# Performance work log

Hardware: AMD Instinct MI355X
Metric: run time of the kernel (lower is better)

Reference implementation:

```python
import jax, jax.numpy as jnp
import numpy as np

HIDDEN = 32
N_STEPS = 64  # fixed-step RK4 replaces adaptive Dopri5 (same MLP-eval structure)
STD = 0.1     # init_params: Linear weights ~ N(0, 0.1), biases = 0


def _mlp(w1, b1, w2, b2, w3, b3, y):
    # NODE.forward: fc1 -> relu -> fc2 -> relu -> fc3 (t is unused in the source)
    h = jax.nn.relu(y @ w1 + b1)
    h = jax.nn.relu(h @ w2 + b2)
    return h @ w3 + b3


def setup_inputs() -> dict:
    key = jax.random.key(0)
    ks = jax.random.split(key, 8)
    B, D = 131072, 3
    x = jax.random.normal(ks[0], (B, D), dtype=jnp.float32)
    # eval times in (0.1, 1.0], sorted like a posterior-sample schedule
    samples = jnp.sort(
        jax.random.uniform(ks[1], (8, 1), jnp.float32, 0.1, 1.0), axis=0)
    w1 = (STD * jax.random.normal(ks[2], (D, HIDDEN))).astype(jnp.float32)
    b1 = jnp.zeros((HIDDEN,), jnp.float32)
    w2 = (STD * jax.random.normal(ks[3], (HIDDEN, HIDDEN))).astype(jnp.float32)
    b2 = jnp.zeros((HIDDEN,), jnp.float32)
    w3 = (STD * jax.random.normal(ks[4], (HIDDEN, D))).astype(jnp.float32)
    b3 = jnp.zeros((D,), jnp.float32)
    w_out = (STD * jax.random.normal(ks[5], (D, 1))).astype(jnp.float32)
    b_out = jnp.zeros((1,), jnp.float32)
    return {"x": x, "samples": samples, "w1": w1, "b1": b1, "w2": w2,
            "b2": b2, "w3": w3, "b3": b3, "w_out": w_out, "b_out": b_out}


def reference(x, samples, w1, b1, w2, b2, w3, b3, w_out, b_out):
    t_eval = samples[:, 0]                     # (S,)
    max_T = jnp.max(t_eval)
    dt = max_T / N_STEPS

    def step(y, _):
        k1 = _mlp(w1, b1, w2, b2, w3, b3, y)
        k2 = _mlp(w1, b1, w2, b2, w3, b3, y + 0.5 * dt * k1)
        k3 = _mlp(w1, b1, w2, b2, w3, b3, y + 0.5 * dt * k2)
        k4 = _mlp(w1, b1, w2, b2, w3, b3, y + dt * k3)
        y_new = y + (dt / 6.0) * (k1 + 2.0 * k2 + 2.0 * k3 + k4)
        return y_new, y_new

    # traj[i] is the state at time (i+1)*dt; shape (N_STEPS, B, 3)
    _, traj = jax.lax.scan(jax.checkpoint(step), x, jnp.arange(N_STEPS))

    # gather states at the grid step nearest each eval time
    idx = jnp.clip(jnp.round(t_eval / dt).astype(jnp.int32) - 1, 0, N_STEPS - 1)
    y_eval = traj[idx]                         # (S, B, 3)

    # fc_layers readout -> act_vec (S, B, 1)
    return y_eval @ w_out + b_out
```

## Files before the change

kernel.cpp:

```cpp
#include <hip/hip_runtime.h>

#define NSTEPS 64

typedef __attribute__((ext_vector_type(16))) float float16_;
typedef __attribute__((ext_vector_type(2))) __fp16 half2_;
typedef __attribute__((ext_vector_type(8))) __fp16 half8_;

__device__ __forceinline__ half2_ relu_pk_f16(float a, float b) {
    half2_ h = __builtin_amdgcn_cvt_pkrtz(a, b);
    return __builtin_elementwise_max(h, (half2_)(__fp16)0);
}

__global__ __launch_bounds__(256, 3)
void ode_rk4_mfma(const float* __restrict__ x,
                  const float* __restrict__ samples,
                  const float* __restrict__ w1, const float* __restrict__ b1,
                  const float* __restrict__ w2, const float* __restrict__ b2,
                  const float* __restrict__ w3, const float* __restrict__ b3,
                  const float* __restrict__ w_out, const float* __restrict__ b_out,
                  float* __restrict__ out, int B)
{
    const int lane  = threadIdx.x & 63;
    const int w     = threadIdx.x >> 6;
    const int col32 = lane & 31;
    const int half  = lane >> 5;

    const int rowBase = (blockIdx.x * 4 + w) * 32;
    const int row = rowBase + col32;

    auto pi = [](int m) -> int {
        int bb = (m >> 2) & 3;
        return m + ((bb == 1) ? 4 : (bb == 2) ? -4 : 0);
    };

    union { half2_ h2[4]; half8_ h8; } A1;
    {
        int pm = pi(col32);
        if (half == 0) {
            A1.h2[0] = (half2_){(__fp16)w1[0 * 32 + pm], (__fp16)w1[1 * 32 + pm]};
            A1.h2[1] = (half2_){(__fp16)w1[2 * 32 + pm], (__fp16)b1[pm]};
        } else {
            A1.h2[0] = (half2_)(__fp16)0.0f;
            A1.h2[1] = (half2_)(__fp16)0.0f;
        }
        A1.h2[2] = (half2_)(__fp16)0.0f;
        A1.h2[3] = (half2_)(__fp16)0.0f;
    }

    union { half2_ h2[4]; half8_ h8; } W2T1, W2T2;
#pragma unroll
    for (int pp = 0; pp < 4; ++pp) {
        int i1 = half * 8 + 2 * pp;
        W2T1.h2[pp] = (half2_){(__fp16)w2[i1 * 32 + col32], (__fp16)w2[(i1 + 1) * 32 + col32]};
        W2T2.h2[pp] = (half2_){(__fp16)w2[(i1 + 16) * 32 + col32], (__fp16)w2[(i1 + 17) * 32 + col32]};
    }
    float16_ Cb;
#pragma unroll
    for (int r = 0; r < 16; ++r)
        Cb[r] = b2[(r & 3) + 8 * (r >> 2) + 4 * half];

    union { half2_ h2[4]; half8_ h8; } A31, A32;
#pragma unroll
    for (int pp = 0; pp < 4; ++pp) {
        int j0 = 2 * pp;
        int nu0 = 4 * half + (j0 & 3) + 8 * (j0 >> 2);
        if (col32 < 3) {
            A31.h2[pp] = (half2_){(__fp16)w3[nu0 * 3 + col32], (__fp16)w3[(nu0 + 1) * 3 + col32]};
            A32.h2[pp] = (half2_){(__fp16)w3[(nu0 + 16) * 3 + col32], (__fp16)w3[(nu0 + 17) * 3 + col32]};
        } else {
            A31.h2[pp] = (half2_)(__fp16)0.0f;
            A32.h2[pp] = (half2_)(__fp16)0.0f;
        }
    }

    float16_ Zc;
#pragma unroll
    for (int r = 0; r < 16; ++r) Zc[r] = 0.0f;

    const float maxT = samples[7];
    const float dt   = maxT / 64.0f;
    const float dt2  = 0.5f * dt;
    const float dt6  = dt / 6.0f;

    int sidx[8];
    unsigned long long smask = 0ull;
#pragma unroll
    for (int j = 0; j < 8; ++j) {
        int id = (int)rintf(samples[j] / dt) - 1;
        id = id < 0 ? 0 : (id > NSTEPS - 1 ? NSTEPS - 1 : id);
        id = __builtin_amdgcn_readfirstlane(id);
        sidx[j] = id;
        smask |= 1ull << id;
    }
    const float wo0 = w_out[0], wo1 = w_out[1], wo2 = w_out[2];
    const float bo  = b_out[0];
    const float b30 = b3[0], b31 = b3[1], b32 = b3[2];

    float y0 = x[(size_t)row * 3 + 0];
    float y1 = x[(size_t)row * 3 + 1];
    float y2 = x[(size_t)row * 3 + 2];

#pragma unroll 1
    for (int s = 0; s < NSTEPS; ++s) {
        float acc0 = 0.f, acc1 = 0.f, acc2 = 0.f;
        float a0 = y0, a1 = y1, a2 = y2;

#pragma unroll
        for (int st = 0; st < 4; ++st) {
            half2_ a01 = __builtin_amdgcn_cvt_pkrtz(a0, a1);
            half2_ a2o = __builtin_amdgcn_cvt_pkrtz(a2, 1.0f);
            union { half2_ h2[4]; half8_ h8; } BL1;
            BL1.h2[0] = a01; BL1.h2[1] = a2o;
            BL1.h2[2] = a01; BL1.h2[3] = a2o;

            float16_ D1 = __builtin_amdgcn_mfma_f32_32x32x16_f16(A1.h8, BL1.h8, Zc, 0, 0, 0);

            union { half2_ h2[4]; half8_ h8; } B1, B2;
#pragma unroll
            for (int pp = 0; pp < 4; ++pp) {
                B1.h2[pp] = relu_pk_f16(D1[2 * pp], D1[2 * pp + 1]);
                B2.h2[pp] = relu_pk_f16(D1[8 + 2 * pp], D1[8 + 2 * pp + 1]);
            }

            float16_ D2 = __builtin_amdgcn_mfma_f32_32x32x16_f16(W2T1.h8, B1.h8,
                          __builtin_amdgcn_mfma_f32_32x32x16_f16(W2T2.h8, B2.h8, Cb, 0, 0, 0), 0, 0, 0);

            union { half2_ h2[4]; half8_ h8; } H1, H2;
#pragma unroll
            for (int pp = 0; pp < 4; ++pp) {
                H1.h2[pp] = relu_pk_f16(D2[2 * pp], D2[2 * pp + 1]);
                H2.h2[pp] = relu_pk_f16(D2[8 + 2 * pp], D2[8 + 2 * pp + 1]);
            }

            float16_ D3 = __builtin_amdgcn_mfma_f32_32x32x16_f16(A32.h8, H2.h8,
                          __builtin_amdgcn_mfma_f32_32x32x16_f16(A31.h8, H1.h8, Zc, 0, 0, 0), 0, 0, 0);

            float t0 = D3[0], u0 = D3[0];
            float t1 = D3[1], u1 = D3[1];
            float t2 = D3[2], u2 = D3[2];
            asm volatile("v_permlane32_swap_b32 %0, %1" : "+v"(t0), "+v"(u0));
            asm volatile("v_permlane32_swap_b32 %0, %1" : "+v"(t1), "+v"(u1));
            asm volatile("v_permlane32_swap_b32 %0, %1" : "+v"(t2), "+v"(u2));
            float k0 = t0 + u0 + b30;
            float k1 = t1 + u1 + b31;
            float k2 = t2 + u2 + b32;

            const float ca = (st == 1 || st == 2) ? 2.0f : 1.0f;
            acc0 = fmaf(ca, k0, acc0); acc1 = fmaf(ca, k1, acc1); acc2 = fmaf(ca, k2, acc2);
            const float ci = (st == 2) ? dt : dt2;
            a0 = fmaf(ci, k0, y0); a1 = fmaf(ci, k1, y1); a2 = fmaf(ci, k2, y2);
        }
        y0 = fmaf(dt6, acc0, y0); y1 = fmaf(dt6, acc1, y1); y2 = fmaf(dt6, acc2, y2);

        if ((smask >> s) & 1ull) {
            if (half == 0) {
#pragma unroll
                for (int j = 0; j < 8; ++j) {
                    if (sidx[j] == s) {
                        out[(size_t)j * B + row] = fmaf(y2, wo2, fmaf(y1, wo1, fmaf(y0, wo0, bo)));
                    }
                }
            }
        }
    }
}

extern "C" void kernel_launch(void* const* d_in, const int* in_sizes, int n_in,
                              void* d_out, int out_size, void* d_ws, size_t ws_size,
                              hipStream_t stream) {
    const float* x       = (const float*)d_in[0];
    const float* samples = (const float*)d_in[1];
    const float* w1      = (const float*)d_in[2];
    const float* b1      = (const float*)d_in[3];
    const float* w2      = (const float*)d_in[4];
    const float* b2      = (const float*)d_in[5];
    const float* w3      = (const float*)d_in[6];
    const float* b3      = (const float*)d_in[7];
    const float* w_out   = (const float*)d_in[8];
    const float* b_out   = (const float*)d_in[9];
    float* out = (float*)d_out;

    const int B = in_sizes[0] / 3;
    const int rowsPerBlock = 128;
    const int grid = (B + rowsPerBlock - 1) / rowsPerBlock;
    ode_rk4_mfma<<<grid, 256, 0, stream>>>(
        x, samples, w1, b1, w2, b2, w3, b3, w_out, b_out, out, B);
}
```

Baseline: 213.0 us.

## Split chained MFMAs into independent pairs and drop permlane swaps in layer 3

```diff
diff --git a/kernel.cpp b/kernel.cpp
--- a/kernel.cpp
+++ b/kernel.cpp
@@ -11,7 +11,7 @@
     return __builtin_elementwise_max(h, (half2_)(__fp16)0);
 }
 
-__global__ __launch_bounds__(256, 3)
+__global__ __launch_bounds__(256, 4)
 void ode_rk4_mfma(const float* __restrict__ x,
                   const float* __restrict__ samples,
                   const float* __restrict__ w1, const float* __restrict__ b1,
@@ -60,16 +60,20 @@
         Cb[r] = b2[(r & 3) + 8 * (r >> 2) + 4 * half];
 
     union { half2_ h2[4]; half8_ h8; } A31, A32;
+    {
+        const bool live = (col32 < 8) && ((col32 & 3) < 3);
+        const int  d    = col32 & 3;
 #pragma unroll
-    for (int pp = 0; pp < 4; ++pp) {
-        int j0 = 2 * pp;
-        int nu0 = 4 * half + (j0 & 3) + 8 * (j0 >> 2);
-        if (col32 < 3) {
-            A31.h2[pp] = (half2_){(__fp16)w3[nu0 * 3 + col32], (__fp16)w3[(nu0 + 1) * 3 + col32]};
-            A32.h2[pp] = (half2_){(__fp16)w3[(nu0 + 16) * 3 + col32], (__fp16)w3[(nu0 + 17) * 3 + col32]};
-        } else {
-            A31.h2[pp] = (half2_)(__fp16)0.0f;
-            A32.h2[pp] = (half2_)(__fp16)0.0f;
+        for (int pp = 0; pp < 4; ++pp) {
+            int j0 = 2 * pp;
+            int nu0 = 4 * half + (j0 & 3) + 8 * (j0 >> 2);
+            if (live) {
+                A31.h2[pp] = (half2_){(__fp16)w3[nu0 * 3 + d], (__fp16)w3[(nu0 + 1) * 3 + d]};
+                A32.h2[pp] = (half2_){(__fp16)w3[(nu0 + 16) * 3 + d], (__fp16)w3[(nu0 + 17) * 3 + d]};
+            } else {
+                A31.h2[pp] = (half2_)(__fp16)0.0f;
+                A32.h2[pp] = (half2_)(__fp16)0.0f;
+            }
         }
     }
 
@@ -122,28 +126,24 @@
                 B2.h2[pp] = relu_pk_f16(D1[8 + 2 * pp], D1[8 + 2 * pp + 1]);
             }
 
-            float16_ D2 = __builtin_amdgcn_mfma_f32_32x32x16_f16(W2T1.h8, B1.h8,
-                          __builtin_amdgcn_mfma_f32_32x32x16_f16(W2T2.h8, B2.h8, Cb, 0, 0, 0), 0, 0, 0);
+            float16_ D2a = __builtin_amdgcn_mfma_f32_32x32x16_f16(W2T1.h8, B1.h8, Cb, 0, 0, 0);
+            float16_ D2b = __builtin_amdgcn_mfma_f32_32x32x16_f16(W2T2.h8, B2.h8, Zc, 0, 0, 0);
 
             union { half2_ h2[4]; half8_ h8; } H1, H2;
 #pragma unroll
             for (int pp = 0; pp < 4; ++pp) {
-                H1.h2[pp] = relu_pk_f16(D2[2 * pp], D2[2 * pp + 1]);
-                H2.h2[pp] = relu_pk_f16(D2[8 + 2 * pp], D2[8 + 2 * pp + 1]);
+                H1.h2[pp] = relu_pk_f16(D2a[2 * pp] + D2b[2 * pp],
+                                        D2a[2 * pp + 1] + D2b[2 * pp + 1]);
+                H2.h2[pp] = relu_pk_f16(D2a[8 + 2 * pp] + D2b[8 + 2 * pp],
+                                        D2a[8 + 2 * pp + 1] + D2b[8 + 2 * pp + 1]);
             }
 
-            float16_ D3 = __builtin_amdgcn_mfma_f32_32x32x16_f16(A32.h8, H2.h8,
-                          __builtin_amdgcn_mfma_f32_32x32x16_f16(A31.h8, H1.h8, Zc, 0, 0, 0), 0, 0, 0);
+            float16_ D3a = __builtin_amdgcn_mfma_f32_32x32x16_f16(A31.h8, H1.h8, Zc, 0, 0, 0);
+            float16_ D3b = __builtin_amdgcn_mfma_f32_32x32x16_f16(A32.h8, H2.h8, Zc, 0, 0, 0);
 
-            float t0 = D3[0], u0 = D3[0];
-            float t1 = D3[1], u1 = D3[1];
-            float t2 = D3[2], u2 = D3[2];
-            asm volatile("v_permlane32_swap_b32 %0, %1" : "+v"(t0), "+v"(u0));
-            asm volatile("v_permlane32_swap_b32 %0, %1" : "+v"(t1), "+v"(u1));
-            asm volatile("v_permlane32_swap_b32 %0, %1" : "+v"(t2), "+v"(u2));
-            float k0 = t0 + u0 + b30;
-            float k1 = t1 + u1 + b31;
-            float k2 = t2 + u2 + b32;
+            float k0 = D3a[0] + D3b[0] + b30;
+            float k1 = D3a[1] + D3b[1] + b31;
+            float k2 = D3a[2] + D3b[2] + b32;
 
             const float ca = (st == 1 || st == 2) ? 2.0f : 1.0f;
             acc0 = fmaf(ca, k0, acc0); acc1 = fmaf(ca, k1, acc1); acc2 = fmaf(ca, k2, acc2);
```

After: 227.2 us. +6.7%, slower.
